# Kernel optimization log

Measured on AMD Instinct MI355X. Metric: run time of the kernel, lower is better.

The kernel has to match this reference:

```python
import jax, jax.numpy as jnp
import numpy as np

LAMBDA = 0.01

def setup_inputs() -> dict:
    key = jax.random.key(0)
    x = jax.random.normal(key, (32, 16384, 64), dtype=jnp.float32)
    return {"x": x}

def reference(x):
    # x: (B, N, D)
    B, N, D = x.shape
    mean = jnp.mean(x, axis=1, keepdims=True)          # (B, 1, D)
    diffs = x - mean                                    # (B, N, D)
    # Fused covariance: sum of centered outer products == GEMM, no (B,N,D,D) blowup
    cov = jnp.einsum('bnd,bne->bde', diffs, diffs) / (N - 1)  # (B, D, D)
    cov = cov + LAMBDA * jnp.eye(D, dtype=x.dtype)
    # torch.unique on the flattened symmetric matrices == globally sorted set of the
    # B * D*(D+1)/2 distinct entries (duplicates only arise from symmetry, prob-1 for
    # continuous inputs). Extract upper triangle per batch, then global sort.
    iu, ju = jnp.triu_indices(D)
    tri = cov[:, iu, ju]                                # (B, d_out)
    d_out = D * (D + 1) // 2
    return jnp.sort(tri.reshape(-1)).reshape(B, d_out)
```

## Files before the change

### kernel.cpp

```cpp
#include <hip/hip_runtime.h>
#include <stdint.h>


#define BATCHES 32
#define NSAMP   16384
#define DIM     64
#define LAMBDA  0.01f
#define NTRI    2080
#define NOUT    (BATCHES * NTRI)

#define CHUNKS_PER_BATCH 32
#define SAMP_PER_BLOCK   (NSAMP / CHUNKS_PER_BATCH)
#define SAMP_PER_WAVE    (SAMP_PER_BLOCK / 4)
#define PARTIAL_STRIDE   2624

#define KEY_SHIFT 14
#define NBUCKET   (1 << 18)
#define SMALL_MAX 64u
#define SORT_CAP  8192

typedef __attribute__((ext_vector_type(4))) float f32x4;
typedef __attribute__((ext_vector_type(8))) short s16x8;

__device__ __forceinline__ uint32_t f32_to_bf16(float f) {
    uint32_t u = __builtin_bit_cast(uint32_t, f);
    return (u + 0x7FFFu + ((u >> 16) & 1u)) >> 16;
}

__device__ __forceinline__ uint32_t sort_key(float v) {
    uint32_t u = __builtin_bit_cast(uint32_t, v);
    return u ^ (uint32_t)(((int32_t)u >> 31) | 0x80000000u);
}

__constant__ const int c_tmi[10] = {0, 0, 0, 0, 1, 1, 1, 2, 2, 3};
__constant__ const int c_tni[10] = {0, 1, 2, 3, 1, 2, 3, 2, 3, 3};

struct CovLds {
    float red[2][64][41];
    float msum_red[4][64];
};

template <typename EpilogueFn>
__device__ __forceinline__ void cov_body(const float* __restrict__ x, CovLds& L,
                                         EpilogueFn epi) {
    const int tid  = threadIdx.x;
    const int wave = tid >> 6;
    const int lane = tid & 63;
    const int b     = blockIdx.x / CHUNKS_PER_BATCH;
    const int chunk = blockIdx.x % CHUNKS_PER_BATCH;
    const int n_start = chunk * SAMP_PER_BLOCK + wave * SAMP_PER_WAVE;

    const int l15  = lane & 15;
    const int quad = lane >> 4;

    const float* xw = x + ((size_t)b * NSAMP + n_start) * DIM
                        + quad * 8 * DIM + l15;

    f32x4 acc[10];
#pragma unroll
    for (int t = 0; t < 10; ++t) acc[t] = (f32x4){0.f, 0.f, 0.f, 0.f};
    float sum_t[4] = {0.f, 0.f, 0.f, 0.f};

    for (int kc = 0; kc < SAMP_PER_WAVE / 32; ++kc) {
        const float* xs = xw + kc * 32 * DIM;
        float v[8][4];
#pragma unroll
        for (int j = 0; j < 8; ++j)
#pragma unroll
            for (int t = 0; t < 4; ++t)
                v[j][t] = xs[j * DIM + t * 16];

#pragma unroll
        for (int j = 0; j < 8; ++j)
#pragma unroll
            for (int t = 0; t < 4; ++t) sum_t[t] += v[j][t];

        s16x8 frag[4];
#pragma unroll
        for (int t = 0; t < 4; ++t) {
            uint32_t pk0 = f32_to_bf16(v[0][t]) | (f32_to_bf16(v[1][t]) << 16);
            uint32_t pk1 = f32_to_bf16(v[2][t]) | (f32_to_bf16(v[3][t]) << 16);
            uint32_t pk2 = f32_to_bf16(v[4][t]) | (f32_to_bf16(v[5][t]) << 16);
            uint32_t pk3 = f32_to_bf16(v[6][t]) | (f32_to_bf16(v[7][t]) << 16);
            frag[t] = __builtin_bit_cast(s16x8, make_uint4(pk0, pk1, pk2, pk3));
        }

        acc[0] = __builtin_amdgcn_mfma_f32_16x16x32_bf16(frag[0], frag[0], acc[0], 0, 0, 0);
        acc[1] = __builtin_amdgcn_mfma_f32_16x16x32_bf16(frag[0], frag[1], acc[1], 0, 0, 0);
        acc[2] = __builtin_amdgcn_mfma_f32_16x16x32_bf16(frag[0], frag[2], acc[2], 0, 0, 0);
        acc[3] = __builtin_amdgcn_mfma_f32_16x16x32_bf16(frag[0], frag[3], acc[3], 0, 0, 0);
        acc[4] = __builtin_amdgcn_mfma_f32_16x16x32_bf16(frag[1], frag[1], acc[4], 0, 0, 0);
        acc[5] = __builtin_amdgcn_mfma_f32_16x16x32_bf16(frag[1], frag[2], acc[5], 0, 0, 0);
        acc[6] = __builtin_amdgcn_mfma_f32_16x16x32_bf16(frag[1], frag[3], acc[6], 0, 0, 0);
        acc[7] = __builtin_amdgcn_mfma_f32_16x16x32_bf16(frag[2], frag[2], acc[7], 0, 0, 0);
        acc[8] = __builtin_amdgcn_mfma_f32_16x16x32_bf16(frag[2], frag[3], acc[8], 0, 0, 0);
        acc[9] = __builtin_amdgcn_mfma_f32_16x16x32_bf16(frag[3], frag[3], acc[9], 0, 0, 0);
    }

#pragma unroll
    for (int t = 0; t < 4; ++t) {
        sum_t[t] += __shfl_xor(sum_t[t], 16, 64);
        sum_t[t] += __shfl_xor(sum_t[t], 32, 64);
    }
    if (lane < 16) {
#pragma unroll
        for (int t = 0; t < 4; ++t) L.msum_red[wave][t * 16 + lane] = sum_t[t];
    }

    __syncthreads();
    if (wave == 1 || wave == 3) {
        int slot = wave >> 1;
#pragma unroll
        for (int t = 0; t < 10; ++t)
#pragma unroll
            for (int r = 0; r < 4; ++r) L.red[slot][lane][t * 4 + r] = acc[t][r];
    }
    __syncthreads();
    if (wave == 0 || wave == 2) {
        int slot = wave >> 1;
#pragma unroll
        for (int t = 0; t < 10; ++t)
#pragma unroll
            for (int r = 0; r < 4; ++r) acc[t][r] += L.red[slot][lane][t * 4 + r];
    }
    __syncthreads();
    if (wave == 2) {
#pragma unroll
        for (int t = 0; t < 10; ++t)
#pragma unroll
            for (int r = 0; r < 4; ++r) L.red[0][lane][t * 4 + r] = acc[t][r];
    }
    __syncthreads();
    if (wave == 0) {
#pragma unroll
        for (int t = 0; t < 10; ++t)
#pragma unroll
            for (int r = 0; r < 4; ++r) acc[t][r] += L.red[0][lane][t * 4 + r];
        float msum_tot = L.msum_red[0][lane] + L.msum_red[1][lane] +
                         L.msum_red[2][lane] + L.msum_red[3][lane];
        epi(b, lane, quad, l15, acc, msum_tot);
    }
}

__global__ __launch_bounds__(256, 3) void cov_kernel_p(const float* __restrict__ x,
                                                       float* __restrict__ partials) {
    __shared__ CovLds L;
    float* Pb = partials + (size_t)blockIdx.x * PARTIAL_STRIDE;
    cov_body(x, L, [&](int b, int lane, int quad, int l15, f32x4* acc, float msum) {
#pragma unroll
        for (int t = 0; t < 10; ++t)
#pragma unroll
            for (int r = 0; r < 4; ++r)
                Pb[t * 256 + r * 64 + lane] = acc[t][r];
        Pb[2560 + lane] = msum;
    });
}

__global__ __launch_bounds__(256, 3) void cov_kernel_a(const float* __restrict__ x,
                                                       float* __restrict__ S,
                                                       float* __restrict__ Msum) {
    __shared__ CovLds L;
    cov_body(x, L, [&](int b, int lane, int quad, int l15, f32x4* acc, float msum) {
        float* Sb = S + b * DIM * DIM;
#pragma unroll
        for (int t = 0; t < 10; ++t) {
            int d0 = c_tmi[t] * 16 + quad * 4;
            int e  = c_tni[t] * 16 + l15;
#pragma unroll
            for (int r = 0; r < 4; ++r)
                atomicAdd(&Sb[(d0 + r) * DIM + e], acc[t][r]);
        }
        atomicAdd(&Msum[b * DIM + lane], msum);
    });
}

__global__ __launch_bounds__(256) void reduce_kernel(const float* __restrict__ partials,
                                                     float* __restrict__ tri,
                                                     uint32_t* __restrict__ hist) {
    __shared__ float msum[DIM];
    const int b = blockIdx.x, tid = threadIdx.x;
    const float* P0 = partials + (size_t)b * CHUNKS_PER_BATCH * PARTIAL_STRIDE;

    float acc10[10];
#pragma unroll
    for (int k = 0; k < 10; ++k) acc10[k] = 0.f;
    float ms = 0.f;
    for (int c = 0; c < CHUNKS_PER_BATCH; ++c) {
        const float* P = P0 + c * PARTIAL_STRIDE;
#pragma unroll
        for (int k = 0; k < 10; ++k) acc10[k] += P[tid + 256 * k];
        if (tid < DIM) ms += P[2560 + tid];
    }
    if (tid < DIM) msum[tid] = ms;
    __syncthreads();

    const int r = tid >> 6, lane = tid & 63, quad = lane >> 4, l15 = lane & 15;
#pragma unroll
    for (int k = 0; k < 10; ++k) {
        int row = c_tmi[k] * 16 + quad * 4 + r;
        int col = c_tni[k] * 16 + l15;
        if (row <= col) {
            float v = (acc10[k] - msum[row] * msum[col] * (1.0f / NSAMP)) * (1.0f / (NSAMP - 1));
            if (row == col) v += LAMBDA;
            int p = row * 64 - (row * (row + 1)) / 2 + col;
            tri[b * NTRI + p] = v;
            atomicAdd(&hist[sort_key(v) >> KEY_SHIFT], 1u);
        }
    }
}

__global__ void finalize_kernel(const float* __restrict__ S,
                                const float* __restrict__ Msum,
                                float* __restrict__ tri,
                                uint32_t* __restrict__ hist) {
    int t = blockIdx.x * blockDim.x + threadIdx.x;
    int b = t >> 12, de = t & 4095, d = de >> 6, e = de & 63;
    if (d > e) return;
    float ssum = S[b * 4096 + d * 64 + e];
    float md = Msum[b * 64 + d], me = Msum[b * 64 + e];
    float v = (ssum - md * me * (1.0f / NSAMP)) * (1.0f / (NSAMP - 1));
    if (d == e) v += LAMBDA;
    int p = d * 64 - (d * (d + 1)) / 2 + e;
    tri[b * NTRI + p] = v;
    atomicAdd(&hist[sort_key(v) >> KEY_SHIFT], 1u);
}

__global__ __launch_bounds__(256) void scanA_kernel(const uint32_t* __restrict__ hist,
                                                    uint32_t* __restrict__ blocksums) {
    __shared__ uint32_t s[256];
    int tid = threadIdx.x;
    s[tid] = hist[blockIdx.x * 256 + tid];
    __syncthreads();
    for (int off = 128; off > 0; off >>= 1) {
        if (tid < off) s[tid] += s[tid + off];
        __syncthreads();
    }
    if (tid == 0) blocksums[blockIdx.x] = s[0];
}

__global__ __launch_bounds__(256) void scanB_kernel(const uint32_t* __restrict__ hist,
                                                    const uint32_t* __restrict__ blocksums,
                                                    uint32_t* __restrict__ offsets,
                                                    uint2* __restrict__ wl_small,
                                                    uint2* __restrict__ wl_large,
                                                    uint32_t* __restrict__ counts) {
    __shared__ uint32_t bs[256];
    __shared__ uint32_t sc[256];
    __shared__ uint32_t base_sh;
    int tid = threadIdx.x, bid = blockIdx.x;

    uint32_t b4[4]; uint32_t s4 = 0;
#pragma unroll
    for (int i = 0; i < 4; ++i) { b4[i] = blocksums[4 * tid + i]; s4 += b4[i]; }
    bs[tid] = s4;
    __syncthreads();
    for (int off = 1; off < 256; off <<= 1) {
        uint32_t a = (tid >= off) ? bs[tid - off] : 0u;
        __syncthreads();
        bs[tid] += a;
        __syncthreads();
    }
    if (tid == (bid >> 2)) {
        uint32_t base = (tid > 0) ? bs[tid - 1] : 0u;
        for (int i = 0; i < (bid & 3); ++i) base += b4[i];
        base_sh = base;
    }

    uint32_t v = hist[bid * 256 + tid];
    sc[tid] = v;
    __syncthreads();
    for (int off = 1; off < 256; off <<= 1) {
        uint32_t a = (tid >= off) ? sc[tid - off] : 0u;
        __syncthreads();
        sc[tid] += a;
        __syncthreads();
    }
    uint32_t excl = base_sh + sc[tid] - v;
    offsets[bid * 256 + tid] = excl;
    if (v >= 2u) {
        if (v <= SMALL_MAX) {
            uint32_t w = atomicAdd(&counts[0], 1u);
            wl_small[w] = make_uint2(excl, v);
        } else {
            uint32_t w = atomicAdd(&counts[1], 1u);
            wl_large[w] = make_uint2(excl, v);
        }
    }
}

__global__ void scatter_kernel(const float* __restrict__ tri,
                               uint32_t* __restrict__ offsets,
                               float* __restrict__ out) {
    int i = blockIdx.x * blockDim.x + threadIdx.x;
    if (i >= NOUT) return;
    float v = tri[i];
    uint32_t pos = atomicAdd(&offsets[sort_key(v) >> KEY_SHIFT], 1u);
    out[pos] = v;
}

__global__ __launch_bounds__(256) void runsort_kernel(float* __restrict__ out,
                                                      const uint2* __restrict__ wl_small,
                                                      const uint2* __restrict__ wl_large,
                                                      const uint32_t* __restrict__ counts) {
    __shared__ float buf[SORT_CAP];

    uint32_t nl = counts[1];
    for (uint32_t w = blockIdx.x; w < nl; w += gridDim.x) {
        uint2 ent = wl_large[w];
        uint32_t start = ent.x, cnt = ent.y;
        if (cnt > SORT_CAP) continue;
        uint32_t m = 1;
        while (m < cnt) m <<= 1;
        for (uint32_t i = threadIdx.x; i < m; i += blockDim.x)
            buf[i] = (i < cnt) ? out[start + i] : __builtin_inff();
        __syncthreads();
        for (uint32_t k = 2; k <= m; k <<= 1) {
            for (uint32_t j = k >> 1; j > 0; j >>= 1) {
                for (uint32_t i = threadIdx.x; i < m; i += blockDim.x) {
                    uint32_t ixj = i ^ j;
                    if (ixj > i) {
                        float a = buf[i], c = buf[ixj];
                        bool up = ((i & k) == 0u);
                        if ((a > c) == up) { buf[i] = c; buf[ixj] = a; }
                    }
                }
                __syncthreads();
            }
        }
        for (uint32_t i = threadIdx.x; i < cnt; i += blockDim.x)
            out[start + i] = buf[i];
        __syncthreads();
    }

    uint32_t ns = counts[0];
    int wave = threadIdx.x >> 6, lane = threadIdx.x & 63;
    for (uint32_t r = blockIdx.x * 4 + wave; r < ns; r += gridDim.x * 4) {
        uint2 e = wl_small[r];
        uint32_t start = e.x, cnt = e.y;
        float v = (lane < (int)cnt) ? out[start + lane] : __builtin_inff();
#pragma unroll
        for (uint32_t k = 2; k <= 64; k <<= 1)
            for (uint32_t j = k >> 1; j > 0; j >>= 1) {
                float p = __shfl_xor(v, (int)j, 64);
                bool keepmin = (((lane & k) == 0u) == ((lane & j) == 0u));
                v = keepmin ? fminf(v, p) : fmaxf(v, p);
            }
        if (lane < (int)cnt) out[start + lane] = v;
    }
}

static void launch_tail(uint32_t* hist, uint32_t* blocksums, uint32_t* offsets,
                        float* tri, uint2* wl_small, uint2* wl_large,
                        uint32_t* counts, float* out, hipStream_t stream) {
    scanA_kernel<<<NBUCKET / 256, 256, 0, stream>>>(hist, blocksums);
    scanB_kernel<<<NBUCKET / 256, 256, 0, stream>>>(hist, blocksums, offsets,
                                                    wl_small, wl_large, counts);
    scatter_kernel<<<(NOUT + 255) / 256, 256, 0, stream>>>(tri, offsets, out);
    runsort_kernel<<<1024, 256, 0, stream>>>(out, wl_small, wl_large, counts);
}

extern "C" void kernel_launch(void* const* d_in, const int* in_sizes, int n_in,
                              void* d_out, int out_size, void* d_ws, size_t ws_size,
                              hipStream_t stream) {
    const float* x = (const float*)d_in[0];
    float* out = (float*)d_out;
    char* ws = (char*)d_ws;

    const size_t NEED_P = 2666560 + (size_t)1024 * PARTIAL_STRIDE * 4;

    if (ws_size >= NEED_P) {
        uint32_t* hist      = (uint32_t*)(ws);
        uint32_t* counts    = (uint32_t*)(ws + 1048576);
        uint32_t* offsets   = (uint32_t*)(ws + 1048640);
        uint32_t* blocksums = (uint32_t*)(ws + 2097216);
        float*    tri       = (float*)(ws + 2101312);
        uint2*    wl_small  = (uint2*)(ws + 2367552);
        uint2*    wl_large  = (uint2*)(ws + 2633792);
        float*    partials  = (float*)(ws + 2666560);

        hipMemsetAsync(d_ws, 0, 1048640, stream);
        cov_kernel_p<<<BATCHES * CHUNKS_PER_BATCH, 256, 0, stream>>>(x, partials);
        reduce_kernel<<<BATCHES, 256, 0, stream>>>(partials, tri, hist);
        launch_tail(hist, blocksums, offsets, tri, wl_small, wl_large, counts, out, stream);
    } else {
        float*    S         = (float*)(ws);
        float*    Msum      = (float*)(ws + 524288);
        uint32_t* hist      = (uint32_t*)(ws + 532480);
        uint32_t* counts    = (uint32_t*)(ws + 1581056);
        uint32_t* offsets   = (uint32_t*)(ws + 1581120);
        uint32_t* blocksums = (uint32_t*)(ws + 2629696);
        float*    tri       = (float*)(ws + 2633792);
        uint2*    wl_small  = (uint2*)(ws + 2900032);
        uint2*    wl_large  = (uint2*)(ws + 3166272);

        hipMemsetAsync(d_ws, 0, 1581120, stream);
        cov_kernel_a<<<BATCHES * CHUNKS_PER_BATCH, 256, 0, stream>>>(x, S, Msum);
        finalize_kernel<<<(BATCHES * 4096) / 256, 256, 0, stream>>>(S, Msum, tri, hist);
        launch_tail(hist, blocksums, offsets, tri, wl_small, wl_large, counts, out, stream);
    }
}
```

Measured before the change: 313.7 us.

## Double-buffer cov loads, fold histogram zeroing into cov kernel, widen reduce grid

```diff
diff --git a/kernel.cpp b/kernel.cpp
--- a/kernel.cpp
+++ b/kernel.cpp
@@ -1,4 +1,5 @@
 #include <hip/hip_runtime.h>
+#include <hip/hip_bf16.h>
 #include <stdint.h>
 
 
@@ -22,14 +23,16 @@
 typedef __attribute__((ext_vector_type(4))) float f32x4;
 typedef __attribute__((ext_vector_type(8))) short s16x8;
 
-__device__ __forceinline__ uint32_t f32_to_bf16(float f) {
-    uint32_t u = __builtin_bit_cast(uint32_t, f);
-    return (u + 0x7FFFu + ((u >> 16) & 1u)) >> 16;
-}
-
 __device__ __forceinline__ uint32_t sort_key(float v) {
     uint32_t u = __builtin_bit_cast(uint32_t, v);
     return u ^ (uint32_t)(((int32_t)u >> 31) | 0x80000000u);
+}
+
+__device__ __forceinline__ uint32_t cvt_pk_bf16(float lo, float hi) {
+    __hip_bfloat162 bb = __float22bfloat162_rn(make_float2(lo, hi));
+    uint32_t u;
+    __builtin_memcpy(&u, &bb, 4);
+    return u;
 }
 
 __constant__ const int c_tmi[10] = {0, 0, 0, 0, 1, 1, 1, 2, 2, 3};
@@ -61,15 +64,18 @@
     for (int t = 0; t < 10; ++t) acc[t] = (f32x4){0.f, 0.f, 0.f, 0.f};
     float sum_t[4] = {0.f, 0.f, 0.f, 0.f};
 
-    for (int kc = 0; kc < SAMP_PER_WAVE / 32; ++kc) {
+    float va[8][4], vb[8][4];
+
+    auto loadit = [&](float (&v)[8][4], int kc) {
         const float* xs = xw + kc * 32 * DIM;
-        float v[8][4];
 #pragma unroll
         for (int j = 0; j < 8; ++j)
 #pragma unroll
             for (int t = 0; t < 4; ++t)
                 v[j][t] = xs[j * DIM + t * 16];
-
+    };
+
+    auto compute = [&](float (&v)[8][4]) {
 #pragma unroll
         for (int j = 0; j < 8; ++j)
 #pragma unroll
@@ -78,10 +84,10 @@
         s16x8 frag[4];
 #pragma unroll
         for (int t = 0; t < 4; ++t) {
-            uint32_t pk0 = f32_to_bf16(v[0][t]) | (f32_to_bf16(v[1][t]) << 16);
-            uint32_t pk1 = f32_to_bf16(v[2][t]) | (f32_to_bf16(v[3][t]) << 16);
-            uint32_t pk2 = f32_to_bf16(v[4][t]) | (f32_to_bf16(v[5][t]) << 16);
-            uint32_t pk3 = f32_to_bf16(v[6][t]) | (f32_to_bf16(v[7][t]) << 16);
+            uint32_t pk0 = cvt_pk_bf16(v[0][t], v[1][t]);
+            uint32_t pk1 = cvt_pk_bf16(v[2][t], v[3][t]);
+            uint32_t pk2 = cvt_pk_bf16(v[4][t], v[5][t]);
+            uint32_t pk3 = cvt_pk_bf16(v[6][t], v[7][t]);
             frag[t] = __builtin_bit_cast(s16x8, make_uint4(pk0, pk1, pk2, pk3));
         }
 
@@ -95,7 +101,16 @@
         acc[7] = __builtin_amdgcn_mfma_f32_16x16x32_bf16(frag[2], frag[2], acc[7], 0, 0, 0);
         acc[8] = __builtin_amdgcn_mfma_f32_16x16x32_bf16(frag[2], frag[3], acc[8], 0, 0, 0);
         acc[9] = __builtin_amdgcn_mfma_f32_16x16x32_bf16(frag[3], frag[3], acc[9], 0, 0, 0);
-    }
+    };
+
+    loadit(va, 0);
+    loadit(vb, 1);
+    compute(va);
+    loadit(va, 2);
+    compute(vb);
+    loadit(vb, 3);
+    compute(va);
+    compute(vb);
 
 #pragma unroll
     for (int t = 0; t < 4; ++t) {
@@ -143,7 +158,12 @@
 }
 
 __global__ __launch_bounds__(256, 3) void cov_kernel_p(const float* __restrict__ x,
-                                                       float* __restrict__ partials) {
+                                                       float* __restrict__ partials,
+                                                       uint32_t* __restrict__ hist,
+                                                       uint32_t* __restrict__ counts) {
+    hist[blockIdx.x * 256 + threadIdx.x] = 0u;
+    if (blockIdx.x == 0 && threadIdx.x < 16) counts[threadIdx.x] = 0u;
+
     __shared__ CovLds L;
     float* Pb = partials + (size_t)blockIdx.x * PARTIAL_STRIDE;
     cov_body(x, L, [&](int b, int lane, int quad, int l15, f32x4* acc, float msum) {
@@ -177,35 +197,34 @@
 __global__ __launch_bounds__(256) void reduce_kernel(const float* __restrict__ partials,
                                                      float* __restrict__ tri,
                                                      uint32_t* __restrict__ hist) {
+    const int b = blockIdx.x / 10, k = blockIdx.x % 10;
+    const int tid = threadIdx.x;
     __shared__ float msum[DIM];
-    const int b = blockIdx.x, tid = threadIdx.x;
     const float* P0 = partials + (size_t)b * CHUNKS_PER_BATCH * PARTIAL_STRIDE;
 
-    float acc10[10];
-#pragma unroll
-    for (int k = 0; k < 10; ++k) acc10[k] = 0.f;
-    float ms = 0.f;
-    for (int c = 0; c < CHUNKS_PER_BATCH; ++c) {
-        const float* P = P0 + c * PARTIAL_STRIDE;
-#pragma unroll
-        for (int k = 0; k < 10; ++k) acc10[k] += P[tid + 256 * k];
-        if (tid < DIM) ms += P[2560 + tid];
-    }
-    if (tid < DIM) msum[tid] = ms;
+    if (tid < DIM) {
+        float ms = 0.f;
+#pragma unroll
+        for (int c = 0; c < CHUNKS_PER_BATCH; ++c)
+            ms += P0[c * PARTIAL_STRIDE + 2560 + tid];
+        msum[tid] = ms;
+    }
+
+    float a = 0.f;
+#pragma unroll
+    for (int c = 0; c < CHUNKS_PER_BATCH; ++c)
+        a += P0[c * PARTIAL_STRIDE + k * 256 + tid];
     __syncthreads();
 
     const int r = tid >> 6, lane = tid & 63, quad = lane >> 4, l15 = lane & 15;
-#pragma unroll
-    for (int k = 0; k < 10; ++k) {
-        int row = c_tmi[k] * 16 + quad * 4 + r;
-        int col = c_tni[k] * 16 + l15;
-        if (row <= col) {
-            float v = (acc10[k] - msum[row] * msum[col] * (1.0f / NSAMP)) * (1.0f / (NSAMP - 1));
-            if (row == col) v += LAMBDA;
-            int p = row * 64 - (row * (row + 1)) / 2 + col;
-            tri[b * NTRI + p] = v;
-            atomicAdd(&hist[sort_key(v) >> KEY_SHIFT], 1u);
-        }
+    const int row = c_tmi[k] * 16 + quad * 4 + r;
+    const int col = c_tni[k] * 16 + l15;
+    if (row <= col) {
+        float v = (a - msum[row] * msum[col] * (1.0f / NSAMP)) * (1.0f / (NSAMP - 1));
+        if (row == col) v += LAMBDA;
+        int p = row * 64 - (row * (row + 1)) / 2 + col;
+        tri[b * NTRI + p] = v;
+        atomicAdd(&hist[sort_key(v) >> KEY_SHIFT], 1u);
     }
 }
 
@@ -378,9 +397,8 @@
         uint2*    wl_large  = (uint2*)(ws + 2633792);
         float*    partials  = (float*)(ws + 2666560);
 
-        hipMemsetAsync(d_ws, 0, 1048640, stream);
-        cov_kernel_p<<<BATCHES * CHUNKS_PER_BATCH, 256, 0, stream>>>(x, partials);
-        reduce_kernel<<<BATCHES, 256, 0, stream>>>(partials, tri, hist);
+        cov_kernel_p<<<BATCHES * CHUNKS_PER_BATCH, 256, 0, stream>>>(x, partials, hist, counts);
+        reduce_kernel<<<BATCHES * 10, 256, 0, stream>>>(partials, tri, hist);
         launch_tail(hist, blocksums, offsets, tri, wl_small, wl_large, counts, out, stream);
     } else {
         float*    S         = (float*)(ws);
@@ -393,7 +411,7 @@
         uint2*    wl_small  = (uint2*)(ws + 2900032);
         uint2*    wl_large  = (uint2*)(ws + 3166272);
 
-        hipMemsetAsync(d_ws, 0, 1581120, stream);
+        (void)hipMemsetAsync(d_ws, 0, 1581120, stream);
         cov_kernel_a<<<BATCHES * CHUNKS_PER_BATCH, 256, 0, stream>>>(x, S, Msum);
         finalize_kernel<<<(BATCHES * 4096) / 256, 256, 0, stream>>>(S, Msum, tri, hist);
         launch_tail(hist, blocksums, offsets, tri, wl_small, wl_large, counts, out, stream);
```

After: 302.8 us. -3.5%, faster.
